# Kernel optimization log

Measured on AMD Instinct MI355X. Metric: run time of the kernel, lower is better.

Reference implementation:

```python
import jax, jax.numpy as jnp
import numpy as np

N = 50000        # nodes
E = 800000       # edges
F_IN = 128       # num_features
H = 256          # hidden_dim
B = 128          # number of graphs (batch_size)
NUM_CLASSES = 10
SCALE = 3        # (r-1)*Lev+1 = 3
NNZ = 1200000    # nnz of multiscale wavelet transform matrix [SCALE*N, N]


def setup_inputs() -> dict:
    key = jax.random.key(0)
    ks = jax.random.split(key, 16)
    x = jax.random.normal(ks[0], (N, F_IN), jnp.float32)
    edge_index = jax.random.randint(ks[1], (2, E), 0, N)
    batch = jnp.sort(jax.random.randint(ks[2], (N,), 0, B))
    d = jax.random.normal(ks[3], (NNZ,), jnp.float32) * 0.1
    rows = jax.random.randint(ks[4], (NNZ,), 0, SCALE * N)
    cols = jax.random.randint(ks[5], (NNZ,), 0, N)
    d_index = jnp.stack([rows, cols])

    def lin(k, fi, fo):
        return jax.random.normal(k, (fi, fo), jnp.float32) * (1.0 / np.sqrt(fi))

    return {
        "x": x,
        "W1": lin(ks[6], F_IN, H), "b1": jnp.zeros((H,), jnp.float32),
        "W2": lin(ks[7], H, H),    "b2": jnp.zeros((H,), jnp.float32),
        "W3": lin(ks[8], H, H),    "b3": jnp.zeros((H,), jnp.float32),
        "fc1_w": lin(ks[9], SCALE * H, H),  "fc1_b": jnp.zeros((H,), jnp.float32),
        "fc2_w": lin(ks[10], H, H // 2),    "fc2_b": jnp.zeros((H // 2,), jnp.float32),
        "fc3_w": lin(ks[11], H // 2, NUM_CLASSES), "fc3_b": jnp.zeros((NUM_CLASSES,), jnp.float32),
        "d": d,
        "edge_index": edge_index,
        "batch": batch,
        "d_index": d_index,
    }


def reference(x, W1, b1, W2, b2, W3, b3, fc1_w, fc1_b, fc2_w, fc2_b,
              fc3_w, fc3_b, d, edge_index, batch, d_index):
    # --- GCN normalization (PyG GCNConv: add self-loops, sym norm) ---
    loops = jnp.arange(N, dtype=edge_index.dtype)
    src = jnp.concatenate([edge_index[0], loops])
    dst = jnp.concatenate([edge_index[1], loops])
    deg = jax.ops.segment_sum(jnp.ones_like(src, jnp.float32), dst, num_segments=N)
    dinv = jax.lax.rsqrt(jnp.maximum(deg, 1.0))  # deg >= 1 due to self-loops
    norm = dinv[src] * dinv[dst]                 # [E+N]

    def gcn(h, W, b):
        m = h @ W                                              # [N, H]
        agg = jax.ops.segment_sum(norm[:, None] * m[src], dst, num_segments=N)
        return agg + b

    h = jax.nn.relu(gcn(x, W1, b1))
    h = jax.nn.relu(gcn(h, W2, b2))
    h = jax.nn.relu(gcn(h, W3, b3))

    # --- MultiScale wavelet transform + per-graph pooling ---
    # sparse [SCALE*N, N] matmul: xt = T @ h
    xt = jax.ops.segment_sum(d[:, None] * h[d_index[1]], d_index[0],
                             num_segments=SCALE * N)           # [SCALE*N, H]
    # pool per (scale, graph): segment id = scale*B + graph_id
    seg = (jnp.arange(SCALE)[:, None] * B + batch[None, :]).reshape(-1)
    pooled = jax.ops.segment_sum(xt, seg, num_segments=SCALE * B)
    pooled = pooled.reshape(SCALE, B, H).transpose(1, 0, 2).reshape(B, SCALE * H)

    # --- FC head (dropout is identity in eval) ---
    z = jax.nn.relu(pooled @ fc1_w + fc1_b)
    z = jax.nn.relu(z @ fc2_w + fc2_b)
    return jax.nn.log_softmax(z @ fc3_w + fc3_b, axis=-1)      # [B, NUM_CLASSES]
```

## Files before the change

### kernel.cpp

```cpp
#include <hip/hip_runtime.h>
#include <hip/hip_bf16.h>

#define GN 50000
#define GE 800000
#define FIN 128
#define GH 256
#define GB 128
#define NCLS 10
#define GSCALE 3
#define GNNZ 1200000
#define NSEG (GSCALE * GB)
#define PAD 16

__global__ __launch_bounds__(256) void deg_count_kernel(const int* __restrict__ dst,
                                                        int* __restrict__ deg) {
  int i = blockIdx.x * 256 + threadIdx.x;
  if (i < GE) atomicAdd(&deg[dst[i]], 1);
}

__global__ __launch_bounds__(256) void dinv_kernel(const int* __restrict__ deg,
                                                   float* __restrict__ dinv) {
  int i = blockIdx.x * 256 + threadIdx.x;
  if (i < GN) dinv[i] = 1.0f / sqrtf((float)(deg[i] + 1));
}

__global__ __launch_bounds__(256) void scan1_kernel(const int* __restrict__ in,
                                                    int* __restrict__ out,
                                                    int* __restrict__ btot, int n) {
  __shared__ int sh[256];
  int b = blockIdx.x, tid = threadIdx.x;
  int i = b * 256 + tid;
  int v = (i < n) ? in[i] : 0;
  sh[tid] = v;
  __syncthreads();
  for (int ofs = 1; ofs < 256; ofs <<= 1) {
    int t = (tid >= ofs) ? sh[tid - ofs] : 0;
    __syncthreads();
    sh[tid] += t;
    __syncthreads();
  }
  if (i < n) out[i] = sh[tid] - v;
  if (tid == 255) btot[b] = sh[255];
}

__global__ __launch_bounds__(256) void scan2_kernel(int* __restrict__ btot, int nb) {
  __shared__ int sh[256];
  int tid = threadIdx.x;
  int v = (tid < nb) ? btot[tid] : 0;
  sh[tid] = v;
  __syncthreads();
  for (int ofs = 1; ofs < 256; ofs <<= 1) {
    int t = (tid >= ofs) ? sh[tid - ofs] : 0;
    __syncthreads();
    sh[tid] += t;
    __syncthreads();
  }
  if (tid < nb) btot[tid] = sh[tid] - v;
}

__global__ __launch_bounds__(256) void scan3_kernel(int* __restrict__ out,
                                                    const int* __restrict__ btot,
                                                    int n, int total) {
  int b = blockIdx.x, tid = threadIdx.x;
  int i = b * 256 + tid;
  if (i < n) out[i] += btot[b];
  if (i == 0) out[n] = total;
}

__global__ __launch_bounds__(256) void exscan_strided_kernel(const int* __restrict__ in,
                                                             int* __restrict__ out,
                                                             int n, int stride) {
  __shared__ int sh[256];
  __shared__ int carry;
  int tid = threadIdx.x;
  if (tid == 0) carry = 0;
  __syncthreads();
  for (int base = 0; base < n; base += 256) {
    int i = base + tid;
    int v = (i < n) ? in[(size_t)i * stride] : 0;
    sh[tid] = v;
    __syncthreads();
    for (int ofs = 1; ofs < 256; ofs <<= 1) {
      int t = (tid >= ofs) ? sh[tid - ofs] : 0;
      __syncthreads();
      sh[tid] += t;
      __syncthreads();
    }
    if (i < n) out[i] = carry + sh[tid] - v;
    int total = sh[255];
    __syncthreads();
    if (tid == 0) carry += total;
    __syncthreads();
  }
  if (tid == 0) out[n] = carry;
}

__global__ __launch_bounds__(256) void csr_fill_kernel(const int* __restrict__ src,
                                                       const int* __restrict__ dst,
                                                       int* __restrict__ cur,
                                                       int* __restrict__ csr_src) {
  int i = blockIdx.x * 256 + threadIdx.x;
  if (i < GE) {
    int j = atomicAdd(&cur[dst[i]], 1);
    csr_src[j] = src[i];
  }
}

__device__ __forceinline__ int seg_of(int row, const int* __restrict__ batch) {
  int sc = row / GN;
  int node = row - sc * GN;
  return sc * GB + batch[node];
}

__global__ __launch_bounds__(256) void seg_cnt_kernel(const int* __restrict__ rows,
                                                      const int* __restrict__ batch,
                                                      int* __restrict__ scnt_p) {
  int i = blockIdx.x * 256 + threadIdx.x;
  if (i < GNNZ) atomicAdd(&scnt_p[(size_t)seg_of(rows[i], batch) * PAD], 1);
}

__global__ __launch_bounds__(256) void scur_init_kernel(const int* __restrict__ soff,
                                                        int* __restrict__ scur_p) {
  int s = blockIdx.x * 256 + threadIdx.x;
  if (s < NSEG) scur_p[(size_t)s * PAD] = soff[s];
}

__global__ __launch_bounds__(256) void seg_fill_kernel(const int* __restrict__ rows,
                                                       const int* __restrict__ cols,
                                                       const float* __restrict__ d,
                                                       const int* __restrict__ batch,
                                                       int* __restrict__ scur_p,
                                                       int* __restrict__ scol,
                                                       float* __restrict__ sd) {
  int i = blockIdx.x * 256 + threadIdx.x;
  if (i < GNNZ) {
    int j = atomicAdd(&scur_p[(size_t)seg_of(rows[i], batch) * PAD], 1);
    scol[j] = cols[i];
    sd[j] = d[i];
  }
}

template <int K>
__global__ __launch_bounds__(256) void gemm2_kernel(const float* __restrict__ A,
                                                    const float* __restrict__ W,
                                                    float* __restrict__ C, int M) {
  __shared__ float As[16][132];
  __shared__ float Bs[16][128];
  int tid = threadIdx.x;
  int col0 = blockIdx.x * 128;
  int row0 = blockIdx.y * 128;
  int tx = tid & 15, ty = tid >> 4;
  float acc[2][2][4][4] = {};
  for (int kk = 0; kk < K; kk += 16) {
    __syncthreads();
#pragma unroll
    for (int l = 0; l < 2; ++l) {
      int idx = tid + l * 256;
      int r = idx >> 2, q = idx & 3;
      int arow = row0 + r; if (arow >= M) arow = M - 1;
      float4 av = *(const float4*)&A[(size_t)arow * K + kk + q * 4];
      As[q * 4 + 0][r] = av.x;
      As[q * 4 + 1][r] = av.y;
      As[q * 4 + 2][r] = av.z;
      As[q * 4 + 3][r] = av.w;
      int bk = idx >> 5, c4 = idx & 31;
      float4 bv = *(const float4*)&W[(size_t)(kk + bk) * GH + col0 + c4 * 4];
      *(float4*)&Bs[bk][c4 * 4] = bv;
    }
    __syncthreads();
#pragma unroll
    for (int k = 0; k < 16; ++k) {
      float4 a0 = *(const float4*)&As[k][ty * 4];
      float4 a1 = *(const float4*)&As[k][64 + ty * 4];
      float4 b0 = *(const float4*)&Bs[k][tx * 4];
      float4 b1 = *(const float4*)&Bs[k][64 + tx * 4];
      float ar[2][4] = {{a0.x, a0.y, a0.z, a0.w}, {a1.x, a1.y, a1.z, a1.w}};
      float br[2][4] = {{b0.x, b0.y, b0.z, b0.w}, {b1.x, b1.y, b1.z, b1.w}};
#pragma unroll
      for (int p = 0; p < 2; ++p)
#pragma unroll
        for (int qq = 0; qq < 2; ++qq)
#pragma unroll
          for (int i = 0; i < 4; ++i)
#pragma unroll
            for (int j = 0; j < 4; ++j)
              acc[p][qq][i][j] += ar[p][i] * br[qq][j];
    }
  }
#pragma unroll
  for (int p = 0; p < 2; ++p)
#pragma unroll
    for (int i = 0; i < 4; ++i) {
      int r = row0 + p * 64 + ty * 4 + i;
      if (r < M) {
#pragma unroll
        for (int qq = 0; qq < 2; ++qq) {
          float4 v = make_float4(acc[p][qq][i][0], acc[p][qq][i][1],
                                 acc[p][qq][i][2], acc[p][qq][i][3]);
          *(float4*)&C[(size_t)r * GH + col0 + qq * 64 + tx * 4] = v;
        }
      }
    }
}

__global__ __launch_bounds__(256) void agg_kernel(const float* __restrict__ m,
                                                  const float* __restrict__ dinv,
                                                  const int* __restrict__ off,
                                                  const int* __restrict__ srcs,
                                                  const float* __restrict__ bias,
                                                  float* __restrict__ out) {
  int node = blockIdx.x * 4 + (threadIdx.x >> 6);
  if (node >= GN) return;
  int lane = threadIdx.x & 63;
  float4 acc = *(const float4*)&bias[lane * 4];
  float di = dinv[node];
  float w0 = di * di;
  float4 mv = *(const float4*)&m[(size_t)node * GH + lane * 4];
  acc.x += w0 * mv.x; acc.y += w0 * mv.y; acc.z += w0 * mv.z; acc.w += w0 * mv.w;
  int e0 = off[node], e1 = off[node + 1];
  int e = e0;
  for (; e + 2 <= e1; e += 2) {
    int s0 = srcs[e], s1 = srcs[e + 1];
    float w0a = di * dinv[s0];
    float w1a = di * dinv[s1];
    float4 v0 = *(const float4*)&m[(size_t)s0 * GH + lane * 4];
    float4 v1 = *(const float4*)&m[(size_t)s1 * GH + lane * 4];
    acc.x += w0a * v0.x + w1a * v1.x;
    acc.y += w0a * v0.y + w1a * v1.y;
    acc.z += w0a * v0.z + w1a * v1.z;
    acc.w += w0a * v0.w + w1a * v1.w;
  }
  if (e < e1) {
    int s = srcs[e];
    float w = di * dinv[s];
    float4 v = *(const float4*)&m[(size_t)s * GH + lane * 4];
    acc.x += w * v.x; acc.y += w * v.y; acc.z += w * v.z; acc.w += w * v.w;
  }
  acc.x = fmaxf(acc.x, 0.f); acc.y = fmaxf(acc.y, 0.f);
  acc.z = fmaxf(acc.z, 0.f); acc.w = fmaxf(acc.w, 0.f);
  *(float4*)&out[(size_t)node * GH + lane * 4] = acc;
}

__global__ __launch_bounds__(256) void pooled_kernel(const float* __restrict__ h,
                                                     const int* __restrict__ soff,
                                                     const int* __restrict__ scol,
                                                     const float* __restrict__ sd,
                                                     float* __restrict__ pooled) {
  __shared__ int lcol[256];
  __shared__ float ld[256];
  int seg = blockIdx.x;
  int j0 = soff[seg], j1 = soff[seg + 1];
  int cnt = j1 - j0;
  int nparts = gridDim.y;
  int per = (cnt + nparts - 1) / nparts;
  int s = j0 + blockIdx.y * per;
  int e = s + per;
  if (e > j1) e = j1;
  int tid = threadIdx.x;
  float acc = 0.f;
  for (int base = s; base < e; base += 256) {
    int nload = e - base;
    if (nload > 256) nload = 256;
    __syncthreads();
    if (tid < nload) {
      lcol[tid] = scol[base + tid];
      ld[tid] = sd[base + tid];
    }
    __syncthreads();
    for (int t = 0; t < nload; ++t) {
      acc += ld[t] * h[(size_t)lcol[t] * GH + tid];
    }
  }
  atomicAdd(&pooled[(size_t)seg * GH + tid], acc);
}

__global__ __launch_bounds__(256) void fc1_kernel(const float* __restrict__ pooled,
                                                  const float* __restrict__ w,
                                                  const float* __restrict__ b,
                                                  float* __restrict__ z1) {
  __shared__ float vin[GSCALE * GH];
  int g = blockIdx.x, tid = threadIdx.x;
#pragma unroll
  for (int it = 0; it < GSCALE; ++it)
    vin[it * GH + tid] = pooled[(size_t)(it * GB + g) * GH + tid];
  __syncthreads();
  float acc = b[tid];
  for (int j = 0; j < GSCALE * GH; ++j) acc += vin[j] * w[(size_t)j * GH + tid];
  z1[(size_t)g * GH + tid] = fmaxf(acc, 0.f);
}

__global__ __launch_bounds__(128) void fc2_kernel(const float* __restrict__ z1,
                                                  const float* __restrict__ w,
                                                  const float* __restrict__ b,
                                                  float* __restrict__ z2) {
  __shared__ float vin[GH];
  int g = blockIdx.x, tid = threadIdx.x;
  vin[tid] = z1[(size_t)g * GH + tid];
  vin[128 + tid] = z1[(size_t)g * GH + 128 + tid];
  __syncthreads();
  float acc = b[tid];
  for (int j = 0; j < GH; ++j) acc += vin[j] * w[(size_t)j * 128 + tid];
  z2[(size_t)g * 128 + tid] = fmaxf(acc, 0.f);
}

__global__ __launch_bounds__(128) void fc3_kernel(const float* __restrict__ z2,
                                                  const float* __restrict__ w,
                                                  const float* __restrict__ b,
                                                  float* __restrict__ out) {
  int g = threadIdx.x;
  float logit[NCLS];
#pragma unroll
  for (int o = 0; o < NCLS; ++o) logit[o] = b[o];
  for (int k = 0; k < 128; ++k) {
    float zv = z2[(size_t)g * 128 + k];
#pragma unroll
    for (int o = 0; o < NCLS; ++o) logit[o] += zv * w[k * NCLS + o];
  }
  float mx = logit[0];
#pragma unroll
  for (int o = 1; o < NCLS; ++o) mx = fmaxf(mx, logit[o]);
  float lse = 0.f;
#pragma unroll
  for (int o = 0; o < NCLS; ++o) lse += expf(logit[o] - mx);
  lse = logf(lse);
#pragma unroll
  for (int o = 0; o < NCLS; ++o) out[(size_t)g * NCLS + o] = logit[o] - mx - lse;
}

static inline size_t alignup(size_t x) { return (x + 1023) & ~(size_t)1023; }

extern "C" void kernel_launch(void* const* d_in, const int* in_sizes, int n_in,
                              void* d_out, int out_size, void* d_ws, size_t ws_size,
                              hipStream_t stream) {
  const float* x      = (const float*)d_in[0];
  const float* W1     = (const float*)d_in[1];
  const float* b1     = (const float*)d_in[2];
  const float* W2     = (const float*)d_in[3];
  const float* b2     = (const float*)d_in[4];
  const float* W3     = (const float*)d_in[5];
  const float* b3     = (const float*)d_in[6];
  const float* fc1w   = (const float*)d_in[7];
  const float* fc1b   = (const float*)d_in[8];
  const float* fc2w   = (const float*)d_in[9];
  const float* fc2b   = (const float*)d_in[10];
  const float* fc3w   = (const float*)d_in[11];
  const float* fc3b   = (const float*)d_in[12];
  const float* dval   = (const float*)d_in[13];
  const int* eidx     = (const int*)d_in[14];
  const int* batch    = (const int*)d_in[15];
  const int* didx     = (const int*)d_in[16];
  float* out          = (float*)d_out;

  const int* esrc = eidx;
  const int* edst = eidx + GE;
  const int* nzrow = didx;
  const int* nzcol = didx + GNNZ;

  char* ws = (char*)d_ws;
  size_t o = 0;
  auto take = [&](size_t bytes) { char* p = ws + o; o += alignup(bytes); return p; };
  int*   deg     = (int*)take(GN * 4);
  int*   off     = (int*)take((GN + 1) * 4);
  int*   cur     = (int*)take(GN * 4);
  int*   btot    = (int*)take(256 * 4);
  float* dinv    = (float*)take(GN * 4);
  int*   csr_src = (int*)take(GE * 4);
  int*   scnt_p  = (int*)take(NSEG * PAD * 4);
  int*   soff    = (int*)take((NSEG + 1) * 4);
  int*   scur_p  = (int*)take(NSEG * PAD * 4);
  int*   scol    = (int*)take((size_t)GNNZ * 4);
  float* sd      = (float*)take((size_t)GNNZ * 4);
  float* mbuf    = (float*)take((size_t)GN * GH * 4);
  float* hA      = (float*)take((size_t)GN * GH * 4);
  float* hB      = (float*)take((size_t)GN * GH * 4);
  float* pooled  = (float*)take((size_t)NSEG * GH * 4);
  float* z1      = (float*)take((size_t)GB * GH * 4);
  float* z2      = (float*)take((size_t)GB * 128 * 4);
  (void)ws_size; (void)n_in; (void)in_sizes; (void)out_size;

  const int NB = (GN + 255) / 256;

  hipMemsetAsync(deg, 0, GN * 4, stream);
  hipMemsetAsync(scnt_p, 0, NSEG * PAD * 4, stream);
  hipMemsetAsync(pooled, 0, (size_t)NSEG * GH * 4, stream);

  deg_count_kernel<<<GE / 256, 256, 0, stream>>>(edst, deg);
  dinv_kernel<<<NB, 256, 0, stream>>>(deg, dinv);
  scan1_kernel<<<NB, 256, 0, stream>>>(deg, off, btot, GN);
  scan2_kernel<<<1, 256, 0, stream>>>(btot, NB);
  scan3_kernel<<<NB, 256, 0, stream>>>(off, btot, GN, GE);
  hipMemcpyAsync(cur, off, GN * 4, hipMemcpyDeviceToDevice, stream);
  csr_fill_kernel<<<GE / 256, 256, 0, stream>>>(esrc, edst, cur, csr_src);

  seg_cnt_kernel<<<(GNNZ + 255) / 256, 256, 0, stream>>>(nzrow, batch, scnt_p);
  exscan_strided_kernel<<<1, 256, 0, stream>>>(scnt_p, soff, NSEG, PAD);
  scur_init_kernel<<<(NSEG + 255) / 256, 256, 0, stream>>>(soff, scur_p);
  seg_fill_kernel<<<(GNNZ + 255) / 256, 256, 0, stream>>>(nzrow, nzcol, dval, batch,
                                                          scur_p, scol, sd);

  dim3 ggrid2(GH / 128, (GN + 127) / 128);
  gemm2_kernel<FIN><<<ggrid2, 256, 0, stream>>>(x, W1, mbuf, GN);
  agg_kernel<<<(GN + 3) / 4, 256, 0, stream>>>(mbuf, dinv, off, csr_src, b1, hA);
  gemm2_kernel<GH><<<ggrid2, 256, 0, stream>>>(hA, W2, mbuf, GN);
  agg_kernel<<<(GN + 3) / 4, 256, 0, stream>>>(mbuf, dinv, off, csr_src, b2, hB);
  gemm2_kernel<GH><<<ggrid2, 256, 0, stream>>>(hB, W3, mbuf, GN);
  agg_kernel<<<(GN + 3) / 4, 256, 0, stream>>>(mbuf, dinv, off, csr_src, b3, hA);

  pooled_kernel<<<dim3(NSEG, 8), 256, 0, stream>>>(hA, soff, scol, sd, pooled);

  fc1_kernel<<<GB, 256, 0, stream>>>(pooled, fc1w, fc1b, z1);
  fc2_kernel<<<GB, 128, 0, stream>>>(z1, fc2w, fc2b, z2);
  fc3_kernel<<<1, 128, 0, stream>>>(z2, fc3w, fc3b, out);
}
```

Measured before the change: 1.153 ms.

## Replace FP32 SIMT GEMMs with split-bf16 MFMA GEMMs

Swaps the FP32 register-tiled GEMM for a matrix-core kernel using bf16 MFMA 16x16x32. To keep roughly FP32 accuracy, each operand is split into hi and lo bf16 parts and three MFMAs are issued per tile (hi*hi, hi*lo, lo*hi). New conversion kernels build the hi/lo activations before each layer and transposed hi/lo weights. This adds extra passes over the activations and more GEMM input traffic, and the hi/lo buffers reuse the hA/hB workspace.

```diff
diff --git a/kernel.cpp b/kernel.cpp
--- a/kernel.cpp
+++ b/kernel.cpp
@@ -11,6 +11,18 @@
 #define GNNZ 1200000
 #define NSEG (GSCALE * GB)
 #define PAD 16
+
+typedef __attribute__((ext_vector_type(8))) short bf16x8;
+typedef __attribute__((ext_vector_type(4))) float f32x4;
+typedef __attribute__((ext_vector_type(8))) unsigned short us8;
+
+__device__ __forceinline__ unsigned short f2bf(float f) {
+  unsigned int u = __float_as_uint(f);
+  return (unsigned short)((u + 0x7FFF + ((u >> 16) & 1)) >> 16);
+}
+__device__ __forceinline__ float bf2f(unsigned short h) {
+  return __uint_as_float(((unsigned int)h) << 16);
+}
 
 __global__ __launch_bounds__(256) void deg_count_kernel(const int* __restrict__ dst,
                                                         int* __restrict__ deg) {
@@ -140,67 +152,105 @@
   }
 }
 
+__global__ __launch_bounds__(256) void cvt_hilo_kernel(const float* __restrict__ x,
+                                                       unsigned short* __restrict__ hi,
+                                                       unsigned short* __restrict__ lo,
+                                                       int n) {
+  int i = blockIdx.x * 256 + threadIdx.x;
+  if (i < (n >> 2)) {
+    float4 v = ((const float4*)x)[i];
+    ushort4 h, l;
+    h.x = f2bf(v.x); l.x = f2bf(v.x - bf2f(h.x));
+    h.y = f2bf(v.y); l.y = f2bf(v.y - bf2f(h.y));
+    h.z = f2bf(v.z); l.z = f2bf(v.z - bf2f(h.z));
+    h.w = f2bf(v.w); l.w = f2bf(v.w - bf2f(h.w));
+    ((ushort4*)hi)[i] = h;
+    ((ushort4*)lo)[i] = l;
+  }
+}
+
 template <int K>
-__global__ __launch_bounds__(256) void gemm2_kernel(const float* __restrict__ A,
-                                                    const float* __restrict__ W,
-                                                    float* __restrict__ C, int M) {
-  __shared__ float As[16][132];
-  __shared__ float Bs[16][128];
+__global__ __launch_bounds__(256) void cvt_wt_kernel(const float* __restrict__ W,
+                                                     unsigned short* __restrict__ wth,
+                                                     unsigned short* __restrict__ wtl) {
+  int idx = blockIdx.x * 256 + threadIdx.x;
+  if (idx < K * GH) {
+    int k = idx / GH, c = idx - k * GH;
+    float f = W[idx];
+    unsigned short h = f2bf(f);
+    wth[(size_t)c * K + k] = h;
+    wtl[(size_t)c * K + k] = f2bf(f - bf2f(h));
+  }
+}
+
+#define LDP 40
+template <int K>
+__global__ __launch_bounds__(256) void gemm_mfma_kernel(
+    const unsigned short* __restrict__ Ah, const unsigned short* __restrict__ Al,
+    const unsigned short* __restrict__ Bth, const unsigned short* __restrict__ Btl,
+    float* __restrict__ C, int M) {
+  __shared__ unsigned short sAh[128 * LDP], sAl[128 * LDP];
+  __shared__ unsigned short sBh[128 * LDP], sBl[128 * LDP];
   int tid = threadIdx.x;
   int col0 = blockIdx.x * 128;
   int row0 = blockIdx.y * 128;
-  int tx = tid & 15, ty = tid >> 4;
-  float acc[2][2][4][4] = {};
-  for (int kk = 0; kk < K; kk += 16) {
+  int wave = tid >> 6, lane = tid & 63;
+  int wr = wave >> 1, wc = wave & 1;
+  int lr = lane & 15;
+  int kg = lane >> 4;
+  f32x4 acc[4][4] = {};
+
+  for (int kk = 0; kk < K; kk += 32) {
     __syncthreads();
 #pragma unroll
     for (int l = 0; l < 2; ++l) {
       int idx = tid + l * 256;
-      int r = idx >> 2, q = idx & 3;
+      int r = idx >> 2;
+      int ko = (idx & 3) * 8;
       int arow = row0 + r; if (arow >= M) arow = M - 1;
-      float4 av = *(const float4*)&A[(size_t)arow * K + kk + q * 4];
-      As[q * 4 + 0][r] = av.x;
-      As[q * 4 + 1][r] = av.y;
-      As[q * 4 + 2][r] = av.z;
-      As[q * 4 + 3][r] = av.w;
-      int bk = idx >> 5, c4 = idx & 31;
-      float4 bv = *(const float4*)&W[(size_t)(kk + bk) * GH + col0 + c4 * 4];
-      *(float4*)&Bs[bk][c4 * 4] = bv;
-    }
-    __syncthreads();
-#pragma unroll
-    for (int k = 0; k < 16; ++k) {
-      float4 a0 = *(const float4*)&As[k][ty * 4];
-      float4 a1 = *(const float4*)&As[k][64 + ty * 4];
-      float4 b0 = *(const float4*)&Bs[k][tx * 4];
-      float4 b1 = *(const float4*)&Bs[k][64 + tx * 4];
-      float ar[2][4] = {{a0.x, a0.y, a0.z, a0.w}, {a1.x, a1.y, a1.z, a1.w}};
-      float br[2][4] = {{b0.x, b0.y, b0.z, b0.w}, {b1.x, b1.y, b1.z, b1.w}};
-#pragma unroll
-      for (int p = 0; p < 2; ++p)
-#pragma unroll
-        for (int qq = 0; qq < 2; ++qq)
-#pragma unroll
-          for (int i = 0; i < 4; ++i)
-#pragma unroll
-            for (int j = 0; j < 4; ++j)
-              acc[p][qq][i][j] += ar[p][i] * br[qq][j];
-    }
-  }
-#pragma unroll
-  for (int p = 0; p < 2; ++p)
-#pragma unroll
-    for (int i = 0; i < 4; ++i) {
-      int r = row0 + p * 64 + ty * 4 + i;
-      if (r < M) {
-#pragma unroll
-        for (int qq = 0; qq < 2; ++qq) {
-          float4 v = make_float4(acc[p][qq][i][0], acc[p][qq][i][1],
-                                 acc[p][qq][i][2], acc[p][qq][i][3]);
-          *(float4*)&C[(size_t)r * GH + col0 + qq * 64 + tx * 4] = v;
-        }
+      size_t ga = (size_t)arow * K + kk + ko;
+      *(us8*)&sAh[r * LDP + ko] = *(const us8*)&Ah[ga];
+      *(us8*)&sAl[r * LDP + ko] = *(const us8*)&Al[ga];
+      size_t gb = (size_t)(col0 + r) * K + kk + ko;
+      *(us8*)&sBh[r * LDP + ko] = *(const us8*)&Bth[gb];
+      *(us8*)&sBl[r * LDP + ko] = *(const us8*)&Btl[gb];
+    }
+    __syncthreads();
+    bf16x8 ah[4], al[4], bh[4], bl[4];
+#pragma unroll
+    for (int mi = 0; mi < 4; ++mi) {
+      int r = wr * 64 + mi * 16 + lr;
+      ah[mi] = *(const bf16x8*)&sAh[r * LDP + kg * 8];
+      al[mi] = *(const bf16x8*)&sAl[r * LDP + kg * 8];
+    }
+#pragma unroll
+    for (int ni = 0; ni < 4; ++ni) {
+      int c = wc * 64 + ni * 16 + lr;
+      bh[ni] = *(const bf16x8*)&sBh[c * LDP + kg * 8];
+      bl[ni] = *(const bf16x8*)&sBl[c * LDP + kg * 8];
+    }
+#pragma unroll
+    for (int mi = 0; mi < 4; ++mi)
+#pragma unroll
+      for (int ni = 0; ni < 4; ++ni) {
+        acc[mi][ni] = __builtin_amdgcn_mfma_f32_16x16x32_bf16(ah[mi], bh[ni], acc[mi][ni], 0, 0, 0);
+        acc[mi][ni] = __builtin_amdgcn_mfma_f32_16x16x32_bf16(ah[mi], bl[ni], acc[mi][ni], 0, 0, 0);
+        acc[mi][ni] = __builtin_amdgcn_mfma_f32_16x16x32_bf16(al[mi], bh[ni], acc[mi][ni], 0, 0, 0);
       }
-    }
+  }
+#pragma unroll
+  for (int mi = 0; mi < 4; ++mi) {
+    int rbase = row0 + wr * 64 + mi * 16 + kg * 4;
+#pragma unroll
+    for (int ni = 0; ni < 4; ++ni) {
+      int c = col0 + wc * 64 + ni * 16 + lr;
+#pragma unroll
+      for (int r4 = 0; r4 < 4; ++r4) {
+        int r = rbase + r4;
+        if (r < M) C[(size_t)r * GH + c] = acc[mi][ni][r4];
+      }
+    }
+  }
 }
 
 __global__ __launch_bounds__(256) void agg_kernel(const float* __restrict__ m,
@@ -370,6 +420,12 @@
   int*   scur_p  = (int*)take(NSEG * PAD * 4);
   int*   scol    = (int*)take((size_t)GNNZ * 4);
   float* sd      = (float*)take((size_t)GNNZ * 4);
+  unsigned short* wt1h = (unsigned short*)take((size_t)FIN * GH * 2);
+  unsigned short* wt1l = (unsigned short*)take((size_t)FIN * GH * 2);
+  unsigned short* wt2h = (unsigned short*)take((size_t)GH * GH * 2);
+  unsigned short* wt2l = (unsigned short*)take((size_t)GH * GH * 2);
+  unsigned short* wt3h = (unsigned short*)take((size_t)GH * GH * 2);
+  unsigned short* wt3l = (unsigned short*)take((size_t)GH * GH * 2);
   float* mbuf    = (float*)take((size_t)GN * GH * 4);
   float* hA      = (float*)take((size_t)GN * GH * 4);
   float* hB      = (float*)take((size_t)GN * GH * 4);
@@ -378,6 +434,13 @@
   float* z2      = (float*)take((size_t)GB * 128 * 4);
   (void)ws_size; (void)n_in; (void)in_sizes; (void)out_size;
 
+  unsigned short* xh  = (unsigned short*)hA;
+  unsigned short* xl  = xh + (size_t)GN * FIN;
+  unsigned short* a2h = (unsigned short*)hB;
+  unsigned short* a2l = a2h + (size_t)GN * GH;
+  unsigned short* a3h = (unsigned short*)hA;
+  unsigned short* a3l = a3h + (size_t)GN * GH;
+
   const int NB = (GN + 255) / 256;
 
   hipMemsetAsync(deg, 0, GN * 4, stream);
@@ -398,12 +461,21 @@
   seg_fill_kernel<<<(GNNZ + 255) / 256, 256, 0, stream>>>(nzrow, nzcol, dval, batch,
                                                           scur_p, scol, sd);
 
-  dim3 ggrid2(GH / 128, (GN + 127) / 128);
-  gemm2_kernel<FIN><<<ggrid2, 256, 0, stream>>>(x, W1, mbuf, GN);
+  cvt_wt_kernel<FIN><<<(FIN * GH + 255) / 256, 256, 0, stream>>>(W1, wt1h, wt1l);
+  cvt_wt_kernel<GH><<<(GH * GH + 255) / 256, 256, 0, stream>>>(W2, wt2h, wt2l);
+  cvt_wt_kernel<GH><<<(GH * GH + 255) / 256, 256, 0, stream>>>(W3, wt3h, wt3l);
+
+  dim3 mgrid(GH / 128, (GN + 127) / 128);
+  cvt_hilo_kernel<<<(GN * FIN / 4 + 255) / 256, 256, 0, stream>>>(x, xh, xl, GN * FIN);
+  gemm_mfma_kernel<FIN><<<mgrid, 256, 0, stream>>>(xh, xl, wt1h, wt1l, mbuf, GN);
   agg_kernel<<<(GN + 3) / 4, 256, 0, stream>>>(mbuf, dinv, off, csr_src, b1, hA);
-  gemm2_kernel<GH><<<ggrid2, 256, 0, stream>>>(hA, W2, mbuf, GN);
+
+  cvt_hilo_kernel<<<(GN * GH / 4 + 255) / 256, 256, 0, stream>>>(hA, a2h, a2l, GN * GH);
+  gemm_mfma_kernel<GH><<<mgrid, 256, 0, stream>>>(a2h, a2l, wt2h, wt2l, mbuf, GN);
   agg_kernel<<<(GN + 3) / 4, 256, 0, stream>>>(mbuf, dinv, off, csr_src, b2, hB);
-  gemm2_kernel<GH><<<ggrid2, 256, 0, stream>>>(hB, W3, mbuf, GN);
+
+  cvt_hilo_kernel<<<(GN * GH / 4 + 255) / 256, 256, 0, stream>>>(hB, a3h, a3l, GN * GH);
+  gemm_mfma_kernel<GH><<<mgrid, 256, 0, stream>>>(a3h, a3l, wt3h, wt3l, mbuf, GN);
   agg_kernel<<<(GN + 3) / 4, 256, 0, stream>>>(mbuf, dinv, off, csr_src, b3, hA);
 
   pooled_kernel<<<dim3(NSEG, 8), 256, 0, stream>>>(hA, soff, scol, sd, pooled);
```

After: 1.047 ms. 9.2% less time.
